# Performance work log

Hardware: AMD Instinct MI355X
Metric: run time of the kernel (lower is better)

The kernel has to match this reference:

```python
import jax, jax.numpy as jnp
import numpy as np

NEIGHBOR_RATE = 0.1  # neighbor_rate init arg
LEAKY_SLOPE = 0.2
NEG_INF = -1.0e9


def setup_inputs() -> dict:
    key = jax.random.key(0)
    k1, k2, k3, k4 = jax.random.split(key, 4)
    B, N, Din, H, hd = 4, 2048, 128, 4, 32  # output_dim = H*hd = 128
    h = jax.random.normal(k1, (B, N, Din), jnp.float32)
    adj = jax.random.uniform(k2, (B, N, N), jnp.float32)
    # stacked per-head params: W[k] in [Din, hd], a[k] in [2*hd]
    w_bound = 1.0 / np.sqrt(Din)
    a_bound = 1.0 / np.sqrt(2 * hd)
    W = jax.random.uniform(k3, (H, Din, hd), jnp.float32, -w_bound, w_bound)
    a = jax.random.uniform(k4, (H, 2 * hd), jnp.float32, -a_bound, a_bound)
    return {"h": h, "adj": adj, "W": W, "a": a}


def reference(h, adj, W, a):
    B, N, _ = h.shape
    H, _, hd = W.shape
    k = int(NEIGHBOR_RATE * N)  # num_neighbors
    # Wh: [B,H,N,hd]
    Wh = jnp.einsum('bnf,hfd->bhnd', h, W)
    # cat([Wh_i, Wh_j]) @ a  ==  Wh_i @ a[:hd] + Wh_j @ a[hd:] (broadcast trick)
    s_i = jnp.einsum('bhnd,hd->bhn', Wh, a[:, :hd])
    s_j = jnp.einsum('bhnd,hd->bhn', Wh, a[:, hd:])
    e = jax.nn.leaky_relu(s_i[..., :, None] + s_j[..., None, :], LEAKY_SLOPE)  # [B,H,N,N]
    # top-k mask along last (neighbor) axis, built by scatter like torch .scatter_
    _, idx = jax.lax.top_k(e, k)  # [B,H,N,k]
    row_mask = lambda i: jnp.zeros((N,), jnp.bool_).at[i].set(True)
    mask = jax.vmap(row_mask)(idx.reshape(-1, k)).reshape(e.shape)
    masked = jnp.where(mask, e, NEG_INF)
    attn = jax.nn.softmax(masked, axis=-1) * adj[:, None]  # [B,H,N,N]
    hp = jnp.einsum('bhnm,bhmd->bhnd', attn, Wh)
    # concat heads on feature dim -> [B,N,H*hd]
    return hp.transpose(0, 2, 1, 3).reshape(B, N, H * hd)
```

## Files before the change

### kernel.cpp

```cpp
#include <hip/hip_runtime.h>
#include <hip/hip_bf16.h>
#include <cmath>

#define BB 4
#define NN 2048
#define DIN 128
#define HH 4
#define HD 32
#define KSEL 204
#define BH (BB*HH)
#define KPAD 256
#define KST 264

typedef __attribute__((ext_vector_type(8))) short short8;
typedef __attribute__((ext_vector_type(4))) short short4v;
typedef __attribute__((ext_vector_type(4))) float float4v;

static __device__ inline short f2bf(float x) {
    __hip_bfloat16 b = __float2bfloat16(x);
    return __builtin_bit_cast(short, b);
}

__global__ __launch_bounds__(256) void s_kernel(const float* __restrict__ h,
                                                const float* __restrict__ W,
                                                const float* __restrict__ a,
                                                float* __restrict__ si, float* __restrict__ sj) {
    __shared__ float w1L[HH][DIN], w2L[HH][DIN];
    int t = threadIdx.x;
    for (int e = t; e < 8 * DIN; e += 256) {
        int f = e & 127, v = e >> 7;
        int hh = v >> 1, half = v & 1;
        const float* Wp = W + ((size_t)hh * DIN + f) * HD;
        const float* ap = a + hh * 64 + half * 32;
        float acc = 0.f;
#pragma unroll
        for (int d = 0; d < 32; ++d) acc += Wp[d] * ap[d];
        if (half == 0) w1L[hh][f] = acc; else w2L[hh][f] = acc;
    }
    __syncthreads();

    int gid = blockIdx.x * 256 + t;
    int row = gid >> 2;
    int q   = gid & 3;
    int b = row >> 11, n = row & 2047;
    const float* hr = h + (size_t)row * DIN;

    float s1h0 = 0.f, s1h1 = 0.f, s1h2 = 0.f, s1h3 = 0.f;
    float s2h0 = 0.f, s2h1 = 0.f, s2h2 = 0.f, s2h3 = 0.f;
#pragma unroll
    for (int i = 0; i < 8; ++i) {
        int f = q * 4 + i * 16;
        float4 x = *(const float4*)(hr + f);
        const float* wa0 = &w1L[0][f]; const float* wb0 = &w2L[0][f];
        const float* wa1 = &w1L[1][f]; const float* wb1 = &w2L[1][f];
        const float* wa2 = &w1L[2][f]; const float* wb2 = &w2L[2][f];
        const float* wa3 = &w1L[3][f]; const float* wb3 = &w2L[3][f];
        s1h0 += x.x*wa0[0] + x.y*wa0[1] + x.z*wa0[2] + x.w*wa0[3];
        s2h0 += x.x*wb0[0] + x.y*wb0[1] + x.z*wb0[2] + x.w*wb0[3];
        s1h1 += x.x*wa1[0] + x.y*wa1[1] + x.z*wa1[2] + x.w*wa1[3];
        s2h1 += x.x*wb1[0] + x.y*wb1[1] + x.z*wb1[2] + x.w*wb1[3];
        s1h2 += x.x*wa2[0] + x.y*wa2[1] + x.z*wa2[2] + x.w*wa2[3];
        s2h2 += x.x*wb2[0] + x.y*wb2[1] + x.z*wb2[2] + x.w*wb2[3];
        s1h3 += x.x*wa3[0] + x.y*wa3[1] + x.z*wa3[2] + x.w*wa3[3];
        s2h3 += x.x*wb3[0] + x.y*wb3[1] + x.z*wb3[2] + x.w*wb3[3];
    }
#pragma unroll
    for (int off = 1; off <= 2; off <<= 1) {
        s1h0 += __shfl_xor(s1h0, off); s2h0 += __shfl_xor(s2h0, off);
        s1h1 += __shfl_xor(s1h1, off); s2h1 += __shfl_xor(s2h1, off);
        s1h2 += __shfl_xor(s1h2, off); s2h2 += __shfl_xor(s2h2, off);
        s1h3 += __shfl_xor(s1h3, off); s2h3 += __shfl_xor(s2h3, off);
    }
    float o1 = (q == 0) ? s1h0 : (q == 1) ? s1h1 : (q == 2) ? s1h2 : s1h3;
    float o2 = (q == 0) ? s2h0 : (q == 1) ? s2h1 : (q == 2) ? s2h2 : s2h3;
    size_t o = (size_t)(b * HH + q) * NN + n;
    si[o] = o1; sj[o] = o2;
}

__global__ __launch_bounds__(1024) void select_kernel(
        const float* __restrict__ h, const float* __restrict__ W,
        const float* __restrict__ sj,
        int* __restrict__ idxsel, float* __restrict__ sjsel,
        float* __restrict__ sjmax, short* __restrict__ Whsel) {
    int bh = blockIdx.x;
    int b = bh >> 2, hh = bh & 3;
    int t = threadIdx.x, lane = t & 63, w = t >> 6;
    __shared__ float sv[NN];
    __shared__ short WT[32][136];
    __shared__ int hist16[16][256];
    __shared__ int binInfo[2];
    __shared__ int wtot[4];
    __shared__ int wtotg[16], wtote[16], woffg[16], woffe[16];
    __shared__ float wmax[16];
    __shared__ int idxLDS[KSEL];

    for (int e = t; e < 32 * 128; e += 1024) {
        int n = e >> 7, k = e & 127;
        WT[n][k] = f2bf(W[(size_t)hh * (DIN * HD) + k * HD + n]);
    }

    const float* s = sj + (size_t)bh * NN;
    int j0 = t * 2;
    float2 xx = *(const float2*)(s + j0);
    sv[j0] = xx.x; sv[j0 + 1] = xx.y;
    unsigned u0 = __builtin_bit_cast(unsigned, xx.x);
    unsigned u1 = __builtin_bit_cast(unsigned, xx.y);
    u0 = (u0 & 0x80000000u) ? ~u0 : (u0 | 0x80000000u);
    u1 = (u1 & 0x80000000u) ? ~u1 : (u1 | 0x80000000u);
    float lmax = fmaxf(xx.x, xx.y);
#pragma unroll
    for (int off = 32; off >= 1; off >>= 1) lmax = fmaxf(lmax, __shfl_xor(lmax, off));
    if (lane == 0) wmax[w] = lmax;
    __syncthreads();
    if (t == 0) {
        float m = wmax[0];
#pragma unroll
        for (int i = 1; i < 16; ++i) m = fmaxf(m, wmax[i]);
        sjmax[bh] = m;
    }

    unsigned prefix = 0;
    int need = KSEL;
#pragma unroll
    for (int shift = 24; shift >= 0; shift -= 8) {
        ((int*)hist16)[t] = 0; ((int*)hist16)[t + 1024] = 0;
        ((int*)hist16)[t + 2048] = 0; ((int*)hist16)[t + 3072] = 0;
        __syncthreads();
        unsigned hmask = (shift < 24) ? (0xFFFFFFFFu << (shift + 8)) : 0u;
        if (((u0 ^ prefix) & hmask) == 0) atomicAdd(&hist16[w][(u0 >> shift) & 255], 1);
        if (((u1 ^ prefix) & hmask) == 0) atomicAdd(&hist16[w][(u1 >> shift) & 255], 1);
        __syncthreads();
        int sc = 0, hv = 0, bb = 0;
        if (t < 256) {
            bb = 255 - t;
            hv = 0;
#pragma unroll
            for (int i = 0; i < 16; ++i) hv += hist16[i][bb];
            sc = hv;
#pragma unroll
            for (int off = 1; off < 64; off <<= 1) {
                int u = __shfl_up(sc, off);
                if (lane >= off) sc += u;
            }
            if (lane == 63) wtot[w] = sc;
        }
        __syncthreads();
        if (t < 256) {
            int woffset = 0;
#pragma unroll
            for (int i = 0; i < 4; ++i) woffset += (i < w) ? wtot[i] : 0;
            int incl = sc + woffset;
            int excl = incl - hv;
            if (incl >= need && excl < need) {
                binInfo[0] = bb;
                binInfo[1] = excl;
            }
        }
        __syncthreads();
        prefix |= ((unsigned)binInfo[0]) << shift;
        need -= binInfo[1];
        __syncthreads();
    }
    unsigned T = prefix;
    int n_gt = KSEL - need;

    int cg = (u0 > T ? 1 : 0) + (u1 > T ? 1 : 0);
    int ce = (u0 == T ? 1 : 0) + (u1 == T ? 1 : 0);
    int sg = cg, se = ce;
#pragma unroll
    for (int off = 1; off < 64; off <<= 1) {
        int ug = __shfl_up(sg, off), ue = __shfl_up(se, off);
        if (lane >= off) { sg += ug; se += ue; }
    }
    if (lane == 63) { wtotg[w] = sg; wtote[w] = se; }
    __syncthreads();
    if (t == 0) {
        int rg = 0, re = 0;
#pragma unroll
        for (int i = 0; i < 16; ++i) {
            woffg[i] = rg; rg += wtotg[i];
            woffe[i] = re; re += wtote[i];
        }
    }
    __syncthreads();
    int pg = woffg[w] + sg - cg;
    int te = woffe[w] + se - ce;
    {
        unsigned kk[2] = {u0, u1};
#pragma unroll
        for (int r = 0; r < 2; ++r) {
            int j = j0 + r;
            if (kk[r] > T) {
                idxsel[bh * KSEL + pg] = j;
                sjsel[bh * KSEL + pg] = sv[j];
                idxLDS[pg] = j;
                pg++;
            } else if (kk[r] == T) {
                if (te < need) {
                    int pos = n_gt + te;
                    idxsel[bh * KSEL + pos] = j;
                    sjsel[bh * KSEL + pos] = sv[j];
                    idxLDS[pos] = j;
                }
                te++;
            }
        }
    }
    __syncthreads();

    {
        int mr = lane & 15, quad = lane >> 4;
        int jjp = w * 16 + mr;
        bool valid = jjp < KSEL;
        const float* hrow = h + ((size_t)b * NN + (valid ? idxLDS[jjp] : 0)) * DIN + quad * 8;
        float4v acc0 = {0.f, 0.f, 0.f, 0.f};
        float4v acc1 = {0.f, 0.f, 0.f, 0.f};
#pragma unroll
        for (int ks = 0; ks < 4; ++ks) {
            short8 afr;
            if (valid) {
                float4 xa = *(const float4*)(hrow + ks * 32);
                float4 xb = *(const float4*)(hrow + ks * 32 + 4);
                afr[0] = f2bf(xa.x); afr[1] = f2bf(xa.y); afr[2] = f2bf(xa.z); afr[3] = f2bf(xa.w);
                afr[4] = f2bf(xb.x); afr[5] = f2bf(xb.y); afr[6] = f2bf(xb.z); afr[7] = f2bf(xb.w);
            } else {
                afr = (short8){0, 0, 0, 0, 0, 0, 0, 0};
            }
            short8 b0 = *(const short8*)&WT[mr][ks * 32 + quad * 8];
            short8 b1 = *(const short8*)&WT[16 + mr][ks * 32 + quad * 8];
            acc0 = __builtin_amdgcn_mfma_f32_16x16x32_bf16(afr, b0, acc0, 0, 0, 0);
            acc1 = __builtin_amdgcn_mfma_f32_16x16x32_bf16(afr, b1, acc1, 0, 0, 0);
        }
        short4v o0, o1;
#pragma unroll
        for (int r = 0; r < 4; ++r) { o0[r] = f2bf(acc0[r]); o1[r] = f2bf(acc1[r]); }
        size_t base = (size_t)bh * HD * KPAD;
        int jjs = w * 16 + quad * 4;
        *(short4v*)&Whsel[base + (size_t)mr * KPAD + jjs] = o0;
        *(short4v*)&Whsel[base + (size_t)(16 + mr) * KPAD + jjs] = o1;
    }
}

__global__ __launch_bounds__(256) void attn2_kernel(
        const float* __restrict__ adj, const float* __restrict__ si,
        const int* __restrict__ idxsel, const float* __restrict__ sjsel,
        const float* __restrict__ sjmax, const short* __restrict__ Whsel,
        float* __restrict__ out) {
    int b = blockIdx.x >> 7;
    int tile = blockIdx.x & 127;
    __shared__ float adjbuf[2][2][NN];
    __shared__ short PSb[HH][16][KST];
    __shared__ int   idxS[HH][KPAD];
    __shared__ float sjS[HH][KPAD];
    __shared__ float invZS[HH][16];
    __shared__ float smaxS[HH];
    int t = threadIdx.x, w = t >> 6, lane = t & 63;
    int mr = lane & 15, quad = lane >> 4;

    int i0 = tile * 16;
    const float* adjb = adj + (size_t)b * NN * NN + (size_t)i0 * NN;

    float4 pre[4];
    {
        const float4* src = (const float4*)adjb;
#pragma unroll
        for (int q = 0; q < 4; ++q) pre[q] = src[q * 256 + t];
    }

    for (int e = t; e < HH * KPAD; e += 256) {
        int hh = e >> 8, jj = e & 255;
        bool v = jj < KSEL;
        idxS[hh][jj] = v ? idxsel[(b * HH + hh) * KSEL + jj] : 0;
        sjS[hh][jj]  = v ? sjsel[(b * HH + hh) * KSEL + jj] : -1e30f;
    }
    if (t < HH) smaxS[t] = sjmax[b * HH + t];

    short8 bfr[2][8];
    {
        const short* wp = Whsel + (size_t)((b * HH + w) * HD) * KPAD;
#pragma unroll
        for (int ni = 0; ni < 2; ++ni)
#pragma unroll
            for (int ks = 0; ks < 8; ++ks)
                bfr[ni][ks] = *(const short8*)(wp + (size_t)(ni * 16 + mr) * KPAD + ks * 32 + quad * 8);
    }

    {
        float4* dst = (float4*)(&adjbuf[0][0][0]);
#pragma unroll
        for (int q = 0; q < 4; ++q) dst[q * 256 + t] = pre[q];
    }
    __syncthreads();

    int bh = b * HH + w;
    float smax = smaxS[w];
    for (int s = 0; s < 8; ++s) {
        if (s < 7) {
            const float4* src = (const float4*)(adjb + (size_t)(s + 1) * 2 * NN);
#pragma unroll
            for (int q = 0; q < 4; ++q) pre[q] = src[q * 256 + t];
        }
#pragma unroll
        for (int r = 0; r < 2; ++r) {
            int i_loc = s * 2 + r;
            float siv = si[(size_t)bh * NN + i0 + i_loc];
            float m = siv + smax;
            m = (m >= 0.f) ? m : 0.2f * m;
            float z = 0.f;
            short* prow = &PSb[w][i_loc][0];
#pragma unroll
            for (int k = 0; k < 2; ++k) {
                int jj = k * 128 + lane * 2;
                int ja = idxS[w][jj], jb = idxS[w][jj + 1];
                float ava = adjbuf[s & 1][r][ja], avb = adjbuf[s & 1][r][jb];
                float ea = siv + sjS[w][jj];
                float eb = siv + sjS[w][jj + 1];
                ea = (ea >= 0.f) ? ea : 0.2f * ea;
                eb = (eb >= 0.f) ? eb : 0.2f * eb;
                float ca = __expf(ea - m);
                float cb = __expf(eb - m);
                z += ca + cb;
                short2 p;
                p.x = f2bf(ca * ava);
                p.y = f2bf(cb * avb);
                *(short2*)&prow[jj] = p;
            }
#pragma unroll
            for (int off = 32; off >= 1; off >>= 1) z += __shfl_xor(z, off);
            if (lane == 0) invZS[w][i_loc] = 1.0f / z;
        }
        if (s < 7) {
            float4* dst = (float4*)(&adjbuf[(s + 1) & 1][0][0]);
#pragma unroll
            for (int q = 0; q < 4; ++q) dst[q * 256 + t] = pre[q];
        }
        __syncthreads();
    }
#pragma unroll
    for (int ni = 0; ni < 2; ++ni) {
        float4v acc = {0.f, 0.f, 0.f, 0.f};
#pragma unroll
        for (int ks = 0; ks < 8; ++ks) {
            short8 afr = *(const short8*)&PSb[w][mr][ks * 32 + quad * 8];
            acc = __builtin_amdgcn_mfma_f32_16x16x32_bf16(afr, bfr[ni][ks], acc, 0, 0, 0);
        }
#pragma unroll
        for (int r = 0; r < 4; ++r) {
            int i_loc = quad * 4 + r;
            int d = ni * 16 + mr;
            out[((size_t)(b * NN + i0 + i_loc)) * (HH * HD) + w * HD + d] =
                acc[r] * invZS[w][i_loc];
        }
    }
}

extern "C" void kernel_launch(void* const* d_in, const int* in_sizes, int n_in,
                              void* d_out, int out_size, void* d_ws, size_t ws_size,
                              hipStream_t stream) {
    const float* h   = (const float*)d_in[0];
    const float* adj = (const float*)d_in[1];
    const float* W   = (const float*)d_in[2];
    const float* a   = (const float*)d_in[3];
    float* out = (float*)d_out;

    float* si     = (float*)d_ws;
    float* sj     = si + (size_t)BH * NN;
    float* sjsel  = sj + (size_t)BH * NN;
    float* sjmax  = sjsel + (size_t)BH * KSEL;
    int*   idxsel = (int*)(sjmax + 16);
    short* Whsel  = (short*)(idxsel + (size_t)BH * KSEL);

    s_kernel<<<128, 256, 0, stream>>>(h, W, a, si, sj);
    select_kernel<<<BH, 1024, 0, stream>>>(h, W, sj, idxsel, sjsel, sjmax, Whsel);
    attn2_kernel<<<BB * 128, 256, 0, stream>>>(adj, si, idxsel, sjsel, sjmax, Whsel, out);
}
```

Measured before the change: 135.1 us.

## Replace double-buffered adj prefetch with single 4-row LDS buffer loads

The attention kernel drops the register-prefetched double buffer of two adj rows per stage. It now loads four adj rows per stage straight into one LDS buffer, with a barrier before and after each load, so there are fewer stages and fewer barriers. The global-memory loads no longer overlap the softmax compute, which risks exposing load latency. The W transpose loop in the select kernel also swaps its index mapping so consecutive threads read contiguous W elements.

```diff
diff --git a/kernel.cpp b/kernel.cpp
--- a/kernel.cpp
+++ b/kernel.cpp
@@ -95,7 +95,7 @@
     __shared__ int idxLDS[KSEL];
 
     for (int e = t; e < 32 * 128; e += 1024) {
-        int n = e >> 7, k = e & 127;
+        int n = e & 31, k = e >> 5;
         WT[n][k] = f2bf(W[(size_t)hh * (DIN * HD) + k * HD + n]);
     }
 
@@ -248,7 +248,7 @@
         float* __restrict__ out) {
     int b = blockIdx.x >> 7;
     int tile = blockIdx.x & 127;
-    __shared__ float adjbuf[2][2][NN];
+    __shared__ float adjbuf[4][NN];
     __shared__ short PSb[HH][16][KST];
     __shared__ int   idxS[HH][KPAD];
     __shared__ float sjS[HH][KPAD];
@@ -257,16 +257,6 @@
     int t = threadIdx.x, w = t >> 6, lane = t & 63;
     int mr = lane & 15, quad = lane >> 4;
 
-    int i0 = tile * 16;
-    const float* adjb = adj + (size_t)b * NN * NN + (size_t)i0 * NN;
-
-    float4 pre[4];
-    {
-        const float4* src = (const float4*)adjb;
-#pragma unroll
-        for (int q = 0; q < 4; ++q) pre[q] = src[q * 256 + t];
-    }
-
     for (int e = t; e < HH * KPAD; e += 256) {
         int hh = e >> 8, jj = e & 255;
         bool v = jj < KSEL;
@@ -285,25 +275,25 @@
                 bfr[ni][ks] = *(const short8*)(wp + (size_t)(ni * 16 + mr) * KPAD + ks * 32 + quad * 8);
     }
 
+    int i0 = tile * 16;
+    const float* adjb = adj + (size_t)b * NN * NN;
     {
-        float4* dst = (float4*)(&adjbuf[0][0][0]);
-#pragma unroll
-        for (int q = 0; q < 4; ++q) dst[q * 256 + t] = pre[q];
+        const float4* src = (const float4*)(adjb + (size_t)i0 * NN);
+        float4* dst = (float4*)adjbuf;
+#pragma unroll
+        for (int q = 0; q < 8; ++q)
+            dst[q * 256 + t] = src[q * 256 + t];
     }
     __syncthreads();
 
     int bh = b * HH + w;
     float smax = smaxS[w];
-    for (int s = 0; s < 8; ++s) {
-        if (s < 7) {
-            const float4* src = (const float4*)(adjb + (size_t)(s + 1) * 2 * NN);
-#pragma unroll
-            for (int q = 0; q < 4; ++q) pre[q] = src[q * 256 + t];
-        }
-#pragma unroll
-        for (int r = 0; r < 2; ++r) {
-            int i_loc = s * 2 + r;
-            float siv = si[(size_t)bh * NN + i0 + i_loc];
+    for (int s = 0; s < 4; ++s) {
+#pragma unroll
+        for (int r = 0; r < 4; ++r) {
+            int i_loc = s * 4 + r;
+            int i = i0 + i_loc;
+            float siv = si[(size_t)bh * NN + i];
             float m = siv + smax;
             m = (m >= 0.f) ? m : 0.2f * m;
             float z = 0.f;
@@ -312,7 +302,7 @@
             for (int k = 0; k < 2; ++k) {
                 int jj = k * 128 + lane * 2;
                 int ja = idxS[w][jj], jb = idxS[w][jj + 1];
-                float ava = adjbuf[s & 1][r][ja], avb = adjbuf[s & 1][r][jb];
+                float ava = adjbuf[r][ja], avb = adjbuf[r][jb];
                 float ea = siv + sjS[w][jj];
                 float eb = siv + sjS[w][jj + 1];
                 ea = (ea >= 0.f) ? ea : 0.2f * ea;
@@ -329,12 +319,15 @@
             for (int off = 32; off >= 1; off >>= 1) z += __shfl_xor(z, off);
             if (lane == 0) invZS[w][i_loc] = 1.0f / z;
         }
-        if (s < 7) {
-            float4* dst = (float4*)(&adjbuf[(s + 1) & 1][0][0]);
-#pragma unroll
-            for (int q = 0; q < 4; ++q) dst[q * 256 + t] = pre[q];
-        }
-        __syncthreads();
+        if (s < 3) {
+            __syncthreads();
+            const float4* src = (const float4*)(adjb + (size_t)(i0 + (s + 1) * 4) * NN);
+            float4* dst = (float4*)adjbuf;
+#pragma unroll
+            for (int q = 0; q < 8; ++q)
+                dst[q * 256 + t] = src[q * 256 + t];
+            __syncthreads();
+        }
     }
 #pragma unroll
     for (int ni = 0; ni < 2; ++ni) {
```

New measurement: 130.1 us. 3.7% less time.

## Stream adj rows directly into LDS with async global_load_lds double buffering

Applied to the files above, without the earlier changes.

Replaces the register-staged adj prefetch (global load to registers, then store to LDS) with direct global-to-LDS 16-byte loads. Two buffers are filled up front and synchronization uses manual vmcnt waits plus raw barriers. The si loads inside the loop are replaced by a single per-wave load and broadcast via shuffle, and the W transpose loop index order is swapped for coalesced global reads. This is meant to cut register pressure and VALU/LDS store work on the critical path, but the hand-written waitcnt/barrier logic is fragile and drops the final trailing barrier.

```diff
diff --git a/kernel.cpp b/kernel.cpp
--- a/kernel.cpp
+++ b/kernel.cpp
@@ -19,6 +19,12 @@
 static __device__ inline short f2bf(float x) {
     __hip_bfloat16 b = __float2bfloat16(x);
     return __builtin_bit_cast(short, b);
+}
+
+typedef __attribute__((address_space(1))) const unsigned gq_t;
+typedef __attribute__((address_space(3))) unsigned lq_t;
+static __device__ inline void gload_lds16(const void* g, void* l) {
+    __builtin_amdgcn_global_load_lds((gq_t*)g, (lq_t*)l, 16, 0, 0);
 }
 
 __global__ __launch_bounds__(256) void s_kernel(const float* __restrict__ h,
@@ -95,7 +101,7 @@
     __shared__ int idxLDS[KSEL];
 
     for (int e = t; e < 32 * 128; e += 1024) {
-        int n = e >> 7, k = e & 127;
+        int n = e & 31, k = e >> 5;
         WT[n][k] = f2bf(W[(size_t)hh * (DIN * HD) + k * HD + n]);
     }
 
@@ -260,13 +266,6 @@
     int i0 = tile * 16;
     const float* adjb = adj + (size_t)b * NN * NN + (size_t)i0 * NN;
 
-    float4 pre[4];
-    {
-        const float4* src = (const float4*)adjb;
-#pragma unroll
-        for (int q = 0; q < 4; ++q) pre[q] = src[q * 256 + t];
-    }
-
     for (int e = t; e < HH * KPAD; e += 256) {
         int hh = e >> 8, jj = e & 255;
         bool v = jj < KSEL;
@@ -284,26 +283,46 @@
             for (int ks = 0; ks < 8; ++ks)
                 bfr[ni][ks] = *(const short8*)(wp + (size_t)(ni * 16 + mr) * KPAD + ks * 32 + quad * 8);
     }
+    int bh = b * HH + w;
+    float sivAll = (lane < 16) ? si[(size_t)bh * NN + i0 + lane] : 0.f;
+
+    __syncthreads();
 
     {
-        float4* dst = (float4*)(&adjbuf[0][0][0]);
-#pragma unroll
-        for (int q = 0; q < 4; ++q) dst[q * 256 + t] = pre[q];
-    }
-    __syncthreads();
-
-    int bh = b * HH + w;
+        int lx = lane << 4;
+#pragma unroll
+        for (int q = 0; q < 4; ++q) {
+            int off = (q << 12) + (w << 10);
+            gload_lds16((const char*)adjb + off + lx, (char*)&adjbuf[0][0][0] + off);
+        }
+        const char* gs1 = (const char*)(adjb + (size_t)2 * NN);
+#pragma unroll
+        for (int q = 0; q < 4; ++q) {
+            int off = (q << 12) + (w << 10);
+            gload_lds16(gs1 + off + lx, (char*)&adjbuf[1][0][0] + off);
+        }
+    }
+    asm volatile("s_waitcnt vmcnt(4)" ::: "memory");
+    __builtin_amdgcn_sched_barrier(0);
+    __builtin_amdgcn_s_barrier();
+
     float smax = smaxS[w];
     for (int s = 0; s < 8; ++s) {
-        if (s < 7) {
-            const float4* src = (const float4*)(adjb + (size_t)(s + 1) * 2 * NN);
-#pragma unroll
-            for (int q = 0; q < 4; ++q) pre[q] = src[q * 256 + t];
+        int cur = s & 1;
+        if (s >= 1 && s < 7) {
+            const char* gs = (const char*)(adjb + (size_t)((s + 1) * 2) * NN);
+            char* lb = (char*)&adjbuf[cur ^ 1][0][0];
+            int lx = lane << 4;
+#pragma unroll
+            for (int q = 0; q < 4; ++q) {
+                int off = (q << 12) + (w << 10);
+                gload_lds16(gs + off + lx, lb + off);
+            }
         }
 #pragma unroll
         for (int r = 0; r < 2; ++r) {
             int i_loc = s * 2 + r;
-            float siv = si[(size_t)bh * NN + i0 + i_loc];
+            float siv = __shfl(sivAll, i_loc);
             float m = siv + smax;
             m = (m >= 0.f) ? m : 0.2f * m;
             float z = 0.f;
@@ -312,7 +331,7 @@
             for (int k = 0; k < 2; ++k) {
                 int jj = k * 128 + lane * 2;
                 int ja = idxS[w][jj], jb = idxS[w][jj + 1];
-                float ava = adjbuf[s & 1][r][ja], avb = adjbuf[s & 1][r][jb];
+                float ava = adjbuf[cur][r][ja], avb = adjbuf[cur][r][jb];
                 float ea = siv + sjS[w][jj];
                 float eb = siv + sjS[w][jj + 1];
                 ea = (ea >= 0.f) ? ea : 0.2f * ea;
@@ -330,11 +349,10 @@
             if (lane == 0) invZS[w][i_loc] = 1.0f / z;
         }
         if (s < 7) {
-            float4* dst = (float4*)(&adjbuf[(s + 1) & 1][0][0]);
-#pragma unroll
-            for (int q = 0; q < 4; ++q) dst[q * 256 + t] = pre[q];
-        }
-        __syncthreads();
+            asm volatile("s_waitcnt vmcnt(0)" ::: "memory");
+            __builtin_amdgcn_sched_barrier(0);
+            __builtin_amdgcn_s_barrier();
+        }
     }
 #pragma unroll
     for (int ni = 0; ni < 2; ++ni) {
```

New measurement: 128.9 us. -4.6%, faster.
